# Optimization experiments

Measured on AMD Instinct MI355X. Metric: run time of the kernel, lower is better.

Reference implementation:

```python
import jax, jax.numpy as jnp
import numpy as np

EMBED_DIM = 1024
NUM_HEADS = 8
HEAD_DIM = EMBED_DIM // NUM_HEADS


def setup_inputs() -> dict:
    key = jax.random.key(0)
    k1, k2, k3, k4, k5 = jax.random.split(key, 5)
    B, N, D = 4, 2048, EMBED_DIM
    scale = 1.0 / np.sqrt(D)
    return {
        "representation": jax.random.normal(k1, (B, N, D), dtype=jnp.float32),
        "W_qkv": jax.random.normal(k2, (D, 3 * D), dtype=jnp.float32) * scale,
        "b_qkv": jnp.zeros((3 * D,), dtype=jnp.float32),
        "W_proj": jax.random.normal(k3, (D, D), dtype=jnp.float32) * scale,
        "b_proj": jnp.zeros((D,), dtype=jnp.float32),
    }


def reference(representation, W_qkv, b_qkv, W_proj, b_proj):
    B, N, D = representation.shape
    H, Hd = NUM_HEADS, HEAD_DIM
    qkv = jnp.einsum("bnd,de->bne", representation, W_qkv) + b_qkv  # [B,N,3D]
    q, k, v = jnp.split(qkv, 3, axis=-1)
    # [B,N,D] -> [B,H,N,Hd]
    split_heads = lambda x: x.reshape(B, N, H, Hd).transpose(0, 2, 1, 3)
    q, k, v = split_heads(q), split_heads(k), split_heads(v)
    dots = jnp.einsum("bhqd,bhkd->bhqk", q, k) * (Hd ** -0.5)  # [B,H,N,N]
    attn = jax.nn.softmax(dots, axis=-1)
    out = jnp.einsum("bhqk,bhkd->bhqd", attn, v)
    out = out.transpose(0, 2, 1, 3).reshape(B, N, D)  # merge heads
    return jnp.einsum("bnd,de->bne", out, W_proj) + b_proj
```

## Files before the change

### kernel.cpp

```cpp
#include <hip/hip_runtime.h>
#include <hip/hip_bf16.h>
#include <cstdint>

typedef unsigned short u16;
typedef __attribute__((ext_vector_type(8))) short short8;
typedef __attribute__((ext_vector_type(4))) float f32x4;
typedef __attribute__((ext_vector_type(4))) unsigned short u16x4;

#define NSEQ 2048
#define DMODEL 1024
#define NH 8
#define HD 128
#define KDIM 1024
#define QSCALE (0.08838834764831845f * 1.4426950408889634f)

__device__ __forceinline__ u16 f2b(float f) {
  __hip_bfloat16 h = __float2bfloat16(f);
  union { __hip_bfloat16 h; u16 u; } cv; cv.h = h; return cv.u;
}
__device__ __forceinline__ f32x4 zero4() { f32x4 z = {0.f, 0.f, 0.f, 0.f}; return z; }

__device__ __forceinline__ void gload_lds16(const u16* g, u16* l) {
  __builtin_amdgcn_global_load_lds(
      (__attribute__((address_space(1))) void*)g,
      (__attribute__((address_space(3))) void*)l, 16, 0, 0);
}

__device__ __forceinline__ int LK(int r) {
  return (r & 0x23) | ((r & 0x0C) << 1) | ((r & 0x10) >> 2);
}

__global__ void cvt_f32_bf16(const float* __restrict__ in, u16* __restrict__ out) {
  const size_t i = ((size_t)blockIdx.x * 256 + threadIdx.x) * 8;
  f32x4 a = *(const f32x4*)&in[i];
  f32x4 b = *(const f32x4*)&in[i + 4];
  short8 o;
#pragma unroll
  for (int j = 0; j < 4; ++j) { o[j] = (short)f2b(a[j]); o[4 + j] = (short)f2b(b[j]); }
  *(short8*)&out[i] = o;
}

__global__ void transpose_k(const float* __restrict__ in, u16* __restrict__ out,
                            int R, int C) {
  __shared__ u16 tile[32][33];
  const int tx = threadIdx.x, ty = threadIdx.y;
  const int c = blockIdx.x * 32 + tx;
  const int r0 = blockIdx.y * 32;
  for (int i = ty; i < 32; i += 8) tile[i][tx] = f2b(in[(size_t)(r0 + i) * C + c]);
  __syncthreads();
  const int oc = r0 + tx;
  const int c0 = blockIdx.x * 32;
  for (int i = ty; i < 32; i += 8) out[(size_t)(c0 + i) * R + oc] = tile[tx][i];
}

template <int MODE>
__global__ __launch_bounds__(256, 3) void gemm128(
    const u16* __restrict__ A, const u16* __restrict__ Bt,
    const float* __restrict__ bias, u16* __restrict__ o0,
    u16* __restrict__ o1, u16* __restrict__ o2, float* __restrict__ of) {
  __shared__ __align__(16) u16 sA[128 * 64];
  __shared__ __align__(16) u16 sB[128 * 64];

  const int tid = threadIdx.x;
  const int lane = tid & 63;
  const int w = tid >> 6;
  const int quad = lane >> 4, ln = lane & 15;
  const int m0 = blockIdx.y * 128, n0 = blockIdx.x * 128;
  const int wm = (w >> 1) * 64, wn = (w & 1) * 64;

  f32x4 acc[4][4];
#pragma unroll
  for (int i = 0; i < 4; ++i)
#pragma unroll
    for (int j = 0; j < 4; ++j) acc[i][j] = zero4();

  const int cbase = w * 4;
  for (int kb = 0; kb < KDIM / 64; ++kb) {
    __syncthreads();
    const int k0 = kb * 64;
#pragma unroll
    for (int i = 0; i < 4; ++i) {
      int c = (cbase + i) * 64 + lane;
      int r = c >> 3, s = c & 7;
      gload_lds16(A + (size_t)(m0 + r) * KDIM + k0 + s * 8, &sA[(cbase + i) * 512]);
      gload_lds16(Bt + (size_t)(n0 + r) * KDIM + k0 + s * 8, &sB[(cbase + i) * 512]);
    }
    __syncthreads();
#pragma unroll
    for (int ks = 0; ks < 2; ++ks) {
      short8 af[4], bf[4];
      const int kc = ks * 4 + quad;
#pragma unroll
      for (int t = 0; t < 4; ++t) {
        af[t] = *(const short8*)&sA[(wm + t * 16 + ln) * 64 + kc * 8];
        bf[t] = *(const short8*)&sB[(wn + t * 16 + ln) * 64 + kc * 8];
      }
#pragma unroll
      for (int mt = 0; mt < 4; ++mt)
#pragma unroll
        for (int nt = 0; nt < 4; ++nt)
          acc[mt][nt] = __builtin_amdgcn_mfma_f32_16x16x32_bf16(
              af[mt], bf[nt], acc[mt][nt], 0, 0, 0);
    }
  }

  if (MODE == 0) {
    const int which = n0 >> 10;
    const int h = (n0 & 1023) >> 7;
#pragma unroll
    for (int mt = 0; mt < 4; ++mt) {
      const int rbase = m0 + wm + mt * 16 + quad * 4;
      const int b = rbase >> 11;
      const int n = rbase & 2047;
#pragma unroll
      for (int nt = 0; nt < 4; ++nt) {
        const int dcol = wn + nt * 16 + ln;
        const float bv = bias[n0 + dcol];
        if (which == 0) {
          u16* p = o0 + ((size_t)(b * NH + h) * NSEQ + n) * HD + dcol;
#pragma unroll
          for (int rr = 0; rr < 4; ++rr)
            p[(size_t)rr * HD] = f2b((acc[mt][nt][rr] + bv) * QSCALE);
        } else if (which == 1) {
          u16* p = o1 + ((size_t)(b * NH + h) * NSEQ + n) * HD + dcol;
#pragma unroll
          for (int rr = 0; rr < 4; ++rr)
            p[(size_t)rr * HD] = f2b(acc[mt][nt][rr] + bv);
        } else {
          u16x4 pk;
#pragma unroll
          for (int rr = 0; rr < 4; ++rr) pk[rr] = f2b(acc[mt][nt][rr] + bv);
          *(u16x4*)&o2[((size_t)(b * NH + h) * HD + dcol) * NSEQ + n] = pk;
        }
      }
    }
  } else {
#pragma unroll
    for (int mt = 0; mt < 4; ++mt) {
      const int rbase = m0 + wm + mt * 16 + quad * 4;
#pragma unroll
      for (int nt = 0; nt < 4; ++nt) {
        const int col = n0 + wn + nt * 16 + ln;
        const float bv = bias[col];
#pragma unroll
        for (int rr = 0; rr < 4; ++rr)
          of[(size_t)(rbase + rr) * DMODEL + col] = acc[mt][nt][rr] + bv;
      }
    }
  }
}

__global__ __launch_bounds__(256, 2) void attn_fused(
    const u16* __restrict__ Q, const u16* __restrict__ K,
    const u16* __restrict__ Vt, u16* __restrict__ AO) {
  __shared__ __align__(16) u16 sK[2][64 * 128];
  __shared__ __align__(16) u16 sV[2][128 * 64];

  const int tid = threadIdx.x;
  const int w = tid >> 6, lane = tid & 63;
  const int quad = lane >> 4, ln = lane & 15;
  const int bh = blockIdx.y;
  const int q0 = blockIdx.x * 128;

  const u16* Qb = Q + ((size_t)bh * NSEQ + q0) * HD;
  const u16* Kb = K + (size_t)bh * NSEQ * HD;
  const u16* Vb = Vt + (size_t)bh * HD * NSEQ;

  int gk_off[4], gv_off[4];
#pragma unroll
  for (int j = 0; j < 4; ++j) {
    const int c = (w * 4 + j) * 64 + lane;
    const int rk = c >> 4, sk_ = c & 15;
    gk_off[j] = LK(rk) * HD + (sk_ ^ (rk & 7)) * 8;
    const int rv = c >> 3, sv_ = c & 7;
    gv_off[j] = rv * NSEQ + (sv_ ^ (rv & 7)) * 8;
  }

  short8 qf[2][4];
#pragma unroll
  for (int mt = 0; mt < 2; ++mt)
#pragma unroll
    for (int ks = 0; ks < 4; ++ks)
      qf[mt][ks] = *(const short8*)&Qb[(size_t)(w * 32 + mt * 16 + ln) * HD +
                                       ks * 32 + quad * 8];

  f32x4 o[2][8];
#pragma unroll
  for (int mt = 0; mt < 2; ++mt)
#pragma unroll
    for (int dt = 0; dt < 8; ++dt) o[mt][dt] = zero4();
  float l_part[2] = {0.f, 0.f};

#pragma unroll
  for (int j = 0; j < 4; ++j) {
    gload_lds16(Kb + gk_off[j], &sK[0][(w * 4 + j) * 512]);
    gload_lds16(Vb + gv_off[j], &sV[0][(w * 4 + j) * 512]);
  }

  int cur = 0;
  for (int kv = 0; kv < NSEQ; kv += 64) {
    __syncthreads();

    if (kv + 64 < NSEQ) {
#pragma unroll
      for (int j = 0; j < 4; ++j) {
        gload_lds16(Kb + (size_t)(kv + 64) * HD + gk_off[j],
                    &sK[cur ^ 1][(w * 4 + j) * 512]);
        gload_lds16(Vb + (kv + 64) + gv_off[j],
                    &sV[cur ^ 1][(w * 4 + j) * 512]);
      }
    }

    f32x4 sacc[4][2];
#pragma unroll
    for (int n = 0; n < 4; ++n)
#pragma unroll
      for (int mt = 0; mt < 2; ++mt) sacc[n][mt] = zero4();
    __builtin_amdgcn_s_setprio(1);
#pragma unroll
    for (int ks = 0; ks < 4; ++ks) {
      short8 kf[4];
#pragma unroll
      for (int n = 0; n < 4; ++n)
        kf[n] = *(const short8*)
            &sK[cur][(n * 16 + ln) * 128 + ((((ks << 2) | quad)) ^ (ln & 7)) * 8];
#pragma unroll
      for (int n = 0; n < 4; ++n)
#pragma unroll
        for (int mt = 0; mt < 2; ++mt)
          sacc[n][mt] = __builtin_amdgcn_mfma_f32_16x16x32_bf16(
              kf[n], qf[mt][ks], sacc[n][mt], 0, 0, 0);
    }
    __builtin_amdgcn_s_setprio(0);

    short8 pf[2][2];
#pragma unroll
    for (int mt = 0; mt < 2; ++mt)
#pragma unroll
      for (int ks2 = 0; ks2 < 2; ++ks2) {
        short8 pv;
#pragma unroll
        for (int hf = 0; hf < 2; ++hf)
#pragma unroll
          for (int rr = 0; rr < 4; ++rr) {
            float p = exp2f(sacc[ks2 * 2 + hf][mt][rr]);
            l_part[mt] += p;
            pv[hf * 4 + rr] = (short)f2b(p);
          }
        pf[mt][ks2] = pv;
      }

    __builtin_amdgcn_s_setprio(1);
#pragma unroll
    for (int ks2 = 0; ks2 < 2; ++ks2) {
      short8 vf[8];
#pragma unroll
      for (int dt = 0; dt < 8; ++dt)
        vf[dt] = *(const short8*)
            &sV[cur][(dt * 16 + ln) * 64 + ((((ks2 << 2) | quad)) ^ (ln & 7)) * 8];
#pragma unroll
      for (int mt = 0; mt < 2; ++mt)
#pragma unroll
        for (int dt = 0; dt < 8; ++dt)
          o[mt][dt] = __builtin_amdgcn_mfma_f32_16x16x32_bf16(
              pf[mt][ks2], vf[dt], o[mt][dt], 0, 0, 0);
    }
    __builtin_amdgcn_s_setprio(0);
    cur ^= 1;
  }

  const int b = bh >> 3, h = bh & 7;
#pragma unroll
  for (int mt = 0; mt < 2; ++mt) {
    float v = l_part[mt];
    v += __shfl_xor(v, 16, 64);
    v += __shfl_xor(v, 32, 64);
    float inv[4];
#pragma unroll
    for (int rr = 0; rr < 4; ++rr)
      inv[rr] = 1.0f / __shfl(v, quad * 4 + rr, 64);
    const int rbase = q0 + w * 32 + mt * 16 + quad * 4;
#pragma unroll
    for (int dt = 0; dt < 8; ++dt) {
      const int d = dt * 16 + ln;
#pragma unroll
      for (int rr = 0; rr < 4; ++rr)
        AO[((size_t)b * NSEQ + rbase + rr) * DMODEL + h * HD + d] =
            f2b(o[mt][dt][rr] * inv[rr]);
    }
  }
}

extern "C" void kernel_launch(void* const* d_in, const int* in_sizes, int n_in,
                              void* d_out, int out_size, void* d_ws, size_t ws_size,
                              hipStream_t stream) {
  const float* X = (const float*)d_in[0];
  const float* Wqkv = (const float*)d_in[1];
  const float* bqkv = (const float*)d_in[2];
  const float* Wproj = (const float*)d_in[3];
  const float* bproj = (const float*)d_in[4];
  float* out = (float*)d_out;

  const size_t NEED_BYTES =
      2ull * (8388608  + 3072 * 1024 + 1024 * 1024 + 3 * 8388608 + 8388608);
  if (ws_size < NEED_BYTES) return;

  u16* ws = (u16*)d_ws;
  u16* Xb = ws;
  u16* WqkvT = Xb + 8388608;
  u16* WprojT = WqkvT + 3072 * 1024;
  u16* Qb = WprojT + 1024 * 1024;
  u16* Kb = Qb + 8388608;
  u16* Vtb = Kb + 8388608;
  u16* AO = Vtb + 8388608;

  cvt_f32_bf16<<<8388608 / (256 * 8), 256, 0, stream>>>(X, Xb);
  transpose_k<<<dim3(3072 / 32, 1024 / 32), dim3(32, 8), 0, stream>>>(Wqkv, WqkvT, 1024, 3072);
  transpose_k<<<dim3(1024 / 32, 1024 / 32), dim3(32, 8), 0, stream>>>(Wproj, WprojT, 1024, 1024);
  gemm128<0><<<dim3(3072 / 128, 8192 / 128), 256, 0, stream>>>(
      Xb, WqkvT, bqkv, Qb, Kb, Vtb, nullptr);
  attn_fused<<<dim3(2048 / 128, 32), 256, 0, stream>>>(Qb, Kb, Vtb, AO);
  gemm128<1><<<dim3(1024 / 128, 8192 / 128), 256, 0, stream>>>(
      AO, WprojT, bproj, nullptr, nullptr, nullptr, out);
}
```

Baseline: 273.7 us.

## Interleave softmax exp with QK MFMAs and unroll KV loop by two

Restructures the attention inner loop so the exp2 and bf16 packing of each 16-column score block runs while MFMAs for the next block are issued. The first half of the PV product starts before the last score block is converted. The loop is unrolled by two so buffer indices are compile-time, and LDS fragment offsets are precomputed. bf16 conversion now uses add-0x8000 plus byte-permute rounding (round-half-up rather than round-to-nearest-even), which slightly changes numerics and raises register pressure.

```diff
diff --git a/kernel.cpp b/kernel.cpp
--- a/kernel.cpp
+++ b/kernel.cpp
@@ -6,6 +6,7 @@
 typedef __attribute__((ext_vector_type(8))) short short8;
 typedef __attribute__((ext_vector_type(4))) float f32x4;
 typedef __attribute__((ext_vector_type(4))) unsigned short u16x4;
+typedef __attribute__((ext_vector_type(4))) unsigned int u32x4;
 
 #define NSEQ 2048
 #define DMODEL 1024
@@ -176,6 +177,18 @@
     gv_off[j] = rv * NSEQ + (sv_ ^ (rv & 7)) * 8;
   }
 
+  int kfo[4][4], vfo[2][8];
+#pragma unroll
+  for (int n = 0; n < 4; ++n)
+#pragma unroll
+    for (int ks = 0; ks < 4; ++ks)
+      kfo[n][ks] = (n * 16 + ln) * 128 + ((((ks << 2) | quad) ^ (ln & 7)) * 8);
+#pragma unroll
+  for (int ks2 = 0; ks2 < 2; ++ks2)
+#pragma unroll
+    for (int dt = 0; dt < 8; ++dt)
+      vfo[ks2][dt] = (dt * 16 + ln) * 64 + ((((ks2 << 2) | quad) ^ (ln & 7)) * 8);
+
   short8 qf[2][4];
 #pragma unroll
   for (int mt = 0; mt < 2; ++mt)
@@ -197,76 +210,94 @@
     gload_lds16(Vb + gv_off[j], &sV[0][(w * 4 + j) * 512]);
   }
 
-  int cur = 0;
-  for (int kv = 0; kv < NSEQ; kv += 64) {
-    __syncthreads();
-
-    if (kv + 64 < NSEQ) {
-#pragma unroll
-      for (int j = 0; j < 4; ++j) {
-        gload_lds16(Kb + (size_t)(kv + 64) * HD + gk_off[j],
-                    &sK[cur ^ 1][(w * 4 + j) * 512]);
-        gload_lds16(Vb + (kv + 64) + gv_off[j],
-                    &sV[cur ^ 1][(w * 4 + j) * 512]);
-      }
-    }
-
-    f32x4 sacc[4][2];
-#pragma unroll
-    for (int n = 0; n < 4; ++n)
-#pragma unroll
-      for (int mt = 0; mt < 2; ++mt) sacc[n][mt] = zero4();
-    __builtin_amdgcn_s_setprio(1);
-#pragma unroll
-    for (int ks = 0; ks < 4; ++ks) {
-      short8 kf[4];
-#pragma unroll
-      for (int n = 0; n < 4; ++n)
-        kf[n] = *(const short8*)
-            &sK[cur][(n * 16 + ln) * 128 + ((((ks << 2) | quad)) ^ (ln & 7)) * 8];
-#pragma unroll
-      for (int n = 0; n < 4; ++n)
-#pragma unroll
-        for (int mt = 0; mt < 2; ++mt)
-          sacc[n][mt] = __builtin_amdgcn_mfma_f32_16x16x32_bf16(
-              kf[n], qf[mt][ks], sacc[n][mt], 0, 0, 0);
-    }
-    __builtin_amdgcn_s_setprio(0);
-
-    short8 pf[2][2];
-#pragma unroll
-    for (int mt = 0; mt < 2; ++mt)
-#pragma unroll
-      for (int ks2 = 0; ks2 < 2; ++ks2) {
-        short8 pv;
-#pragma unroll
-        for (int hf = 0; hf < 2; ++hf)
-#pragma unroll
-          for (int rr = 0; rr < 4; ++rr) {
-            float p = exp2f(sacc[ks2 * 2 + hf][mt][rr]);
-            l_part[mt] += p;
-            pv[hf * 4 + rr] = (short)f2b(p);
-          }
-        pf[mt][ks2] = pv;
-      }
-
-    __builtin_amdgcn_s_setprio(1);
-#pragma unroll
-    for (int ks2 = 0; ks2 < 2; ++ks2) {
-      short8 vf[8];
-#pragma unroll
-      for (int dt = 0; dt < 8; ++dt)
-        vf[dt] = *(const short8*)
-            &sV[cur][(dt * 16 + ln) * 64 + ((((ks2 << 2) | quad)) ^ (ln & 7)) * 8];
-#pragma unroll
-      for (int mt = 0; mt < 2; ++mt)
+  union PU { u32x4 u; short8 s; };
+
+#pragma unroll 1
+  for (int it = 0; it < NSEQ / 128; ++it) {
+#pragma unroll
+    for (int c2 = 0; c2 < 2; ++c2) {
+      __syncthreads();
+
+      const int kvn = it * 128 + c2 * 64 + 64;
+      if (kvn < NSEQ) {
+#pragma unroll
+        for (int j = 0; j < 4; ++j) {
+          gload_lds16(Kb + (size_t)kvn * HD + gk_off[j],
+                      &sK[c2 ^ 1][(w * 4 + j) * 512]);
+          gload_lds16(Vb + kvn + gv_off[j], &sV[c2 ^ 1][(w * 4 + j) * 512]);
+        }
+      }
+      const u16* skr = &sK[c2][0];
+      const u16* svr = &sV[c2][0];
+
+      __builtin_amdgcn_s_setprio(1);
+
+      f32x4 sacc[4][2];
+      PU ph[2][2];
+
+      auto SM = [&](int m) {
+#pragma unroll
+        for (int mt = 0; mt < 2; ++mt) {
+          float e0 = exp2f(sacc[m][mt][0]);
+          float e1 = exp2f(sacc[m][mt][1]);
+          float e2 = exp2f(sacc[m][mt][2]);
+          float e3 = exp2f(sacc[m][mt][3]);
+          l_part[mt] += (e0 + e1) + (e2 + e3);
+          unsigned a0 = __float_as_uint(e0) + 0x8000u;
+          unsigned a1 = __float_as_uint(e1) + 0x8000u;
+          unsigned a2 = __float_as_uint(e2) + 0x8000u;
+          unsigned a3 = __float_as_uint(e3) + 0x8000u;
+          ph[mt][m >> 1].u[(m & 1) * 2 + 0] = __builtin_amdgcn_perm(a1, a0, 0x07060302);
+          ph[mt][m >> 1].u[(m & 1) * 2 + 1] = __builtin_amdgcn_perm(a3, a2, 0x07060302);
+        }
+      };
+
+#pragma unroll
+      for (int n = 0; n < 4; ++n) {
+#pragma unroll
+        for (int mt = 0; mt < 2; ++mt) sacc[n][mt] = zero4();
+#pragma unroll
+        for (int ks = 0; ks < 4; ++ks) {
+          short8 kf = *(const short8*)&skr[kfo[n][ks]];
+          sacc[n][0] = __builtin_amdgcn_mfma_f32_16x16x32_bf16(
+              kf, qf[0][ks], sacc[n][0], 0, 0, 0);
+          sacc[n][1] = __builtin_amdgcn_mfma_f32_16x16x32_bf16(
+              kf, qf[1][ks], sacc[n][1], 0, 0, 0);
+        }
+        if (n) SM(n - 1);
+      }
+
+      {
+        short8 pf0 = ph[0][0].s, pf1 = ph[1][0].s;
+        short8 vf[8];
 #pragma unroll
         for (int dt = 0; dt < 8; ++dt)
-          o[mt][dt] = __builtin_amdgcn_mfma_f32_16x16x32_bf16(
-              pf[mt][ks2], vf[dt], o[mt][dt], 0, 0, 0);
-    }
-    __builtin_amdgcn_s_setprio(0);
-    cur ^= 1;
+          vf[dt] = *(const short8*)&svr[vfo[0][dt]];
+#pragma unroll
+        for (int dt = 0; dt < 8; ++dt) {
+          o[0][dt] = __builtin_amdgcn_mfma_f32_16x16x32_bf16(
+              pf0, vf[dt], o[0][dt], 0, 0, 0);
+          o[1][dt] = __builtin_amdgcn_mfma_f32_16x16x32_bf16(
+              pf1, vf[dt], o[1][dt], 0, 0, 0);
+        }
+      }
+      SM(3);
+      {
+        short8 pf0 = ph[0][1].s, pf1 = ph[1][1].s;
+        short8 vf[8];
+#pragma unroll
+        for (int dt = 0; dt < 8; ++dt)
+          vf[dt] = *(const short8*)&svr[vfo[1][dt]];
+#pragma unroll
+        for (int dt = 0; dt < 8; ++dt) {
+          o[0][dt] = __builtin_amdgcn_mfma_f32_16x16x32_bf16(
+              pf0, vf[dt], o[0][dt], 0, 0, 0);
+          o[1][dt] = __builtin_amdgcn_mfma_f32_16x16x32_bf16(
+              pf1, vf[dt], o[1][dt], 0, 0, 0);
+        }
+      }
+      __builtin_amdgcn_s_setprio(0);
+    }
   }
 
   const int b = bh >> 3, h = bh & 7;
```

New measurement: 273.3 us. About the same (-0.1%).
